# Kernel tuning notes

Hardware: AMD Instinct MI355X
Metric: run time of the kernel (lower is better)

The kernel has to match this reference:

```python
import jax, jax.numpy as jnp
import numpy as np

EPS = 1e-12  # F.normalize eps

def _unfold3(x):
    # x: [B,C,H,W] -> [B, C*9, H*W], matching F.unfold(kernel=3, padding=1)
    B, C, H, W = x.shape
    xp = jnp.pad(x, ((0, 0), (0, 0), (1, 1), (1, 1)))
    pats = jnp.stack([xp[:, :, i:i + H, j:j + W]
                      for i in range(3) for j in range(3)], axis=2)  # [B,C,9,H,W]
    return pats.reshape(B, C * 9, H * W)

def _fold3(t, H, W):
    # inverse of _unfold3 with overlap-add, matching F.fold(kernel=3, padding=1)
    B, CK, L = t.shape
    C = CK // 9
    t = t.reshape(B, C, 3, 3, H, W)
    out = jnp.zeros((B, C, H + 2, W + 2), t.dtype)
    for i in range(3):
        for j in range(3):
            out = out.at[:, :, i:i + H, j:j + W].add(t[:, :, i, j])
    return out[:, :, 1:1 + H, 1:1 + W]

def setup_inputs() -> dict:
    key = jax.random.key(0)
    kV, kK, kQ = jax.random.split(key, 3)
    B, C, H, W = 4, 64, 64, 64
    return {
        'V': jax.random.normal(kV, (B, C, H, W), dtype=jnp.float32),
        'K': jax.random.normal(kK, (B, C, H, W), dtype=jnp.float32),
        'Q': jax.random.normal(kQ, (B, C, H, W), dtype=jnp.float32),
    }

def reference(V, K, Q):
    B, C, H, W = Q.shape
    Qu = _unfold3(Q)  # [B, C9, L]
    Ku = _unfold3(K)  # [B, C9, L]
    # F.normalize along the feature (C*9) axis for both K (after permute dim=2) and Q (dim=1)
    Kn = Ku / jnp.maximum(jnp.linalg.norm(Ku, axis=1, keepdims=True), EPS)
    Qn = Qu / jnp.maximum(jnp.linalg.norm(Qu, axis=1, keepdims=True), EPS)
    # R[b,k,q] = <Kn[b,:,k], Qn[b,:,q]>  -> [B, L, L]
    R = jnp.einsum('bfk,bfq->bkq', Kn, Qn)
    S = jnp.max(R, axis=1)        # [B, L]
    arg = jnp.argmax(R, axis=1)   # [B, L] best key patch per query position
    Vu = _unfold3(V)              # [B, C9, L]
    idx = jnp.broadcast_to(arg[:, None, :], Vu.shape)
    T_unfold = jnp.take_along_axis(Vu, idx, axis=2)  # gather along patch dim
    T = _fold3(T_unfold, H, W) / 9.0                 # [B, C, H, W]
    S = S.reshape(B, 1, H, W)
    return (S, T)
```

## Files before the change

kernel.cpp:

```cpp
#include <hip/hip_runtime.h>
#include <math.h>

#define HW 4096

typedef short bf16x8 __attribute__((ext_vector_type(8)));
typedef float floatx4 __attribute__((ext_vector_type(4)));

__device__ __forceinline__ unsigned short f2bf_rne(float x) {
    unsigned int u = __float_as_uint(x);
    unsigned int r = (u + 0x7FFFu + ((u >> 16) & 1u)) >> 16;
    return (unsigned short)r;
}
__device__ __forceinline__ float bf2f(unsigned short h) {
    return __uint_as_float(((unsigned int)h) << 16);
}

__device__ __forceinline__ void gload_lds16(const void* gptr, void* lptr) {
    auto g = (const __attribute__((address_space(1))) unsigned int*)(unsigned long long)(gptr);
    auto l = (__attribute__((address_space(3))) unsigned int*)(unsigned int)(unsigned long long)(lptr);
    __builtin_amdgcn_global_load_lds(g, l, 16, 0, 0);
}

__global__ __launch_bounds__(256)
void prep_kernel(const float* __restrict__ Q, const float* __restrict__ K,
                 unsigned short* __restrict__ Aq, unsigned short* __restrict__ Bq,
                 float* __restrict__ pix2q, float* __restrict__ pix2k) {
    __shared__ float sT[64][65];
    const int tid = threadIdx.x;
    const int p0 = blockIdx.x * 64;
    const int b = blockIdx.y;
    const int pp = tid >> 2, qt = tid & 3;
    const size_t base = ((size_t)b * 4096 + p0 + pp) * 192;

#pragma unroll
    for (int it = 0; it < 16; ++it) {
        int idx = it * 256 + tid;
        int c = idx >> 6, x = idx & 63;
        sT[c][x] = Q[((size_t)b * 64 + c) * HW + p0 + x];
    }
    __syncthreads();
    {
        float sq = 0.f;
#pragma unroll
        for (int i = 0; i < 16; ++i) {
            int c = qt * 16 + i;
            float x = sT[c][pp];
            sq = fmaf(x, x, sq);
            unsigned short h = f2bf_rne(x);
            unsigned short l = f2bf_rne(x - bf2f(h));
            Aq[base + c] = h;
            Aq[base + 64 + c] = h;
            Aq[base + 128 + c] = l;
        }
        sq += __shfl_xor(sq, 1, 64);
        sq += __shfl_xor(sq, 2, 64);
        if (qt == 0) pix2q[(b << 12) + p0 + pp] = sq;
    }
    __syncthreads();

#pragma unroll
    for (int it = 0; it < 16; ++it) {
        int idx = it * 256 + tid;
        int c = idx >> 6, x = idx & 63;
        sT[c][x] = K[((size_t)b * 64 + c) * HW + p0 + x];
    }
    __syncthreads();
    {
        float sk = 0.f;
#pragma unroll
        for (int i = 0; i < 16; ++i) {
            int c = qt * 16 + i;
            float x = sT[c][pp];
            sk = fmaf(x, x, sk);
            unsigned short h = f2bf_rne(x);
            unsigned short l = f2bf_rne(x - bf2f(h));
            Bq[base + c] = h;
            Bq[base + 64 + c] = l;
            Bq[base + 128 + c] = h;
        }
        sk += __shfl_xor(sk, 1, 64);
        sk += __shfl_xor(sk, 2, 64);
        if (qt == 0) pix2k[(b << 12) + p0 + pp] = sk;
    }
}

__global__ void patchnorm_kernel(const float* __restrict__ pix2q, const float* __restrict__ pix2k,
                                 float* __restrict__ rnq, float* __restrict__ rnk) {
    int idx = blockIdx.x * 256 + threadIdx.x;
    int b = idx >> 12, p = idx & 4095;
    int py = p >> 6, px = p & 63;
    float sq = 0.f, sk = 0.f;
    for (int dy = -1; dy <= 1; ++dy)
        for (int dx = -1; dx <= 1; ++dx) {
            int yy = py + dy, xx = px + dx;
            if ((unsigned)yy < 64u && (unsigned)xx < 64u) {
                int o = (b << 12) + (yy << 6) + xx;
                sq += pix2q[o];
                sk += pix2k[o];
            }
        }
    rnq[idx] = 1.f / fmaxf(sqrtf(sq), 1e-12f);
    rnk[idx] = 1.f / fmaxf(sqrtf(sk), 1e-12f);
}

#define WAITV(n_) asm volatile("s_waitcnt vmcnt(" #n_ ")" ::: "memory")
#define PBAR(n_) do { WAITV(n_); __builtin_amdgcn_s_barrier(); \
                      asm volatile("" ::: "memory"); } while (0)

#define ISSUE_CHUNK(g_) do { \
    const int sg_ = (g_) >> 2, r_ = (g_) & 3; \
    _Pragma("unroll") \
    for (int it_ = 0; it_ < 2; ++it_) { \
        int s16_ = it_ * 256 + tid; \
        int rr_ = s16_ >> 3, pos_ = s16_ & 7, G_ = pos_ ^ (rr_ & 7); \
        gload_lds16(ab + (size_t)(r_ * 64 + rr_) * 384 + sg_ * 128 + G_ * 16, \
                    smem + ((r_ * 64 + rr_) * 8 + pos_) * 16); \
        gload_lds16(bb + (size_t)(r_ * 64 + rr_) * 384 + sg_ * 128 + G_ * 16, \
                    smem + 32768 + ((r_ * 64 + rr_) * 8 + pos_) * 16); \
    } \
} while (0)

#define MFMA_STEP(dy_) do { \
    _Pragma("unroll") \
    for (int kk = 0; kk < 2; ++kk) { \
        bf16x8 af[4], bfr[4]; \
        _Pragma("unroll") \
        for (int mt = 0; mt < 4; ++mt) { \
            int row = (dy_) * 64 + wm * 64 + mt * 16 + m15; \
            int pos = (kk * 4 + quad) ^ (row & 7); \
            af[mt] = *(const bf16x8*)(smem + (row * 8 + pos) * 16); \
        } \
        _Pragma("unroll") \
        for (int nt = 0; nt < 4; ++nt) { \
            int row = (dy_) * 64 + wn * 64 + nt * 16 + m15; \
            int pos = (kk * 4 + quad) ^ (row & 7); \
            bfr[nt] = *(const bf16x8*)(smem + 32768 + (row * 8 + pos) * 16); \
        } \
        __builtin_amdgcn_s_setprio(1); \
        _Pragma("unroll") \
        for (int mt = 0; mt < 4; ++mt) \
            _Pragma("unroll") \
            for (int nt = 0; nt < 4; ++nt) \
                acc[mt][nt] = __builtin_amdgcn_mfma_f32_16x16x32_bf16( \
                    af[mt], bfr[nt], acc[mt][nt], 0, 0, 0); \
        __builtin_amdgcn_s_setprio(0); \
    } \
} while (0)

__global__ __launch_bounds__(256, 2)
void gemm_fused_kernel(const unsigned short* __restrict__ Aq, const unsigned short* __restrict__ Bq,
                       const float* __restrict__ rnkA,
                       float* __restrict__ part_val, int* __restrict__ part_arg) {
    __shared__ __align__(16) char smem[65536];
    const int tid = threadIdx.x;
    const int lane = tid & 63, wid = tid >> 6;
    const int m15 = lane & 15, quad = lane >> 4;
    const int wm = wid & 1, wn = wid >> 1;
    const int k0 = blockIdx.x * 128;
    const int q0 = blockIdx.y * 128;
    const int b = blockIdx.z;
    const char* Aqb = (const char*)(Aq + (size_t)b * 4096 * 192);
    const char* Bqb = (const char*)(Bq + (size_t)b * 4096 * 192);
    const bool aInt = (q0 >= 64) && (q0 <= 4096 - 192);
    const bool bInt = (k0 >= 64) && (k0 <= 4096 - 192);

    floatx4 acc[4][4];
#pragma unroll
    for (int i = 0; i < 4; ++i)
#pragma unroll
        for (int j = 0; j < 4; ++j) acc[i][j] = (floatx4)0.f;

    if (aInt && bInt) {
        const char* ab = Aqb + (size_t)(q0 - 64) * 384;
        const char* bb = Bqb + (size_t)(k0 - 64) * 384;
        ISSUE_CHUNK(0); ISSUE_CHUNK(1); ISSUE_CHUNK(2); ISSUE_CHUNK(3);
        PBAR(8);                                MFMA_STEP(0);
        PBAR(4); ISSUE_CHUNK(4);                MFMA_STEP(1);
        PBAR(4); ISSUE_CHUNK(5);                MFMA_STEP(2);
        PBAR(0); ISSUE_CHUNK(6); ISSUE_CHUNK(7); MFMA_STEP(0);
        PBAR(4); ISSUE_CHUNK(8);                MFMA_STEP(1);
        PBAR(4); ISSUE_CHUNK(9);                MFMA_STEP(2);
        PBAR(0); ISSUE_CHUNK(10); ISSUE_CHUNK(11); MFMA_STEP(0);
        PBAR(4);                                MFMA_STEP(1);
        PBAR(0);                                MFMA_STEP(2);
        __syncthreads();
    } else {
        for (int seg = 0; seg < 3; ++seg) {
            const char* abL = Aqb + (size_t)(q0 - 64) * 384 + seg * 128;
            const char* bbL = Bqb + (size_t)(k0 - 64) * 384 + seg * 128;
            if (aInt) {
#pragma unroll
                for (int it = 0; it < 8; ++it) {
                    int slot = it * 256 + tid;
                    int row = slot >> 3, pos = slot & 7;
                    int G = pos ^ (row & 7);
                    gload_lds16(abL + (size_t)row * 384 + G * 16, smem + slot * 16);
                }
            } else {
#pragma unroll
                for (int it = 0; it < 8; ++it) {
                    int slot = it * 256 + tid;
                    int row = slot >> 3, pos = slot & 7;
                    int G = pos ^ (row & 7);
                    uint4 v = make_uint4(0u, 0u, 0u, 0u);
                    if ((unsigned)(q0 - 64 + row) < 4096u)
                        v = *(const uint4*)(abL + (size_t)row * 384 + G * 16);
                    *(uint4*)(smem + slot * 16) = v;
                }
            }
            if (bInt) {
#pragma unroll
                for (int it = 0; it < 8; ++it) {
                    int slot = it * 256 + tid;
                    int row = slot >> 3, pos = slot & 7;
                    int G = pos ^ (row & 7);
                    gload_lds16(bbL + (size_t)row * 384 + G * 16, smem + 32768 + slot * 16);
                }
            } else {
#pragma unroll
                for (int it = 0; it < 8; ++it) {
                    int slot = it * 256 + tid;
                    int row = slot >> 3, pos = slot & 7;
                    int G = pos ^ (row & 7);
                    uint4 v = make_uint4(0u, 0u, 0u, 0u);
                    if ((unsigned)(k0 - 64 + row) < 4096u)
                        v = *(const uint4*)(bbL + (size_t)row * 384 + G * 16);
                    *(uint4*)(smem + 32768 + slot * 16) = v;
                }
            }
            __syncthreads();
            MFMA_STEP(0); MFMA_STEP(1); MFMA_STEP(2);
            __syncthreads();
        }
    }

    float* Csh = (float*)smem;
    float* bvs = (float*)(smem + 34816);
    int*   bas = (int*)(smem + 35840);
    const int q_l = tid & 63;
    const int qr = tid >> 6;
    const int c0 = qr * 32;
    const float4 zero4 = make_float4(0.f, 0.f, 0.f, 0.f);

#pragma unroll
    for (int h = 0; h < 2; ++h) {
        if (h) __syncthreads();
        if (wm == h) {
#pragma unroll
            for (int mt = 0; mt < 4; ++mt)
#pragma unroll
                for (int nt = 0; nt < 4; ++nt)
#pragma unroll
                    for (int j = 0; j < 4; ++j)
                        Csh[(mt * 16 + quad * 4 + j) * 133 + wn * 64 + nt * 16 + m15] =
                            acc[mt][nt][j];
        }
        __syncthreads();

        const bool qm = q_l > 0;
        const bool qp = q_l < 63;
        const float* rC = Csh + q_l * 133;
        const float* rM = Csh + (q_l - 1) * 133;
        const float* rP = Csh + (q_l + 1) * 133;
        float4 prevm = (qm && c0 > 0) ? *(const float4*)&rM[c0 - 4] : zero4;
        float4 rpj   = qp ? *(const float4*)&rP[c0] : zero4;
        float bv = -INFINITY;
        int ba = 0;
#pragma unroll
        for (int j = 0; j < 8; ++j) {
            int c = c0 + 4 * j;
            float4 cen = *(const float4*)&rC[c];
            float4 rm4 = qm ? *(const float4*)&rM[c] : zero4;
            float4 rp1 = (qp && (c + 4) < 128) ? *(const float4*)&rP[c + 4] : zero4;
            float4 o;
            o.x = cen.x + (((c & 63) != 0) ? prevm.w : 0.f) + rpj.y;
            o.y = cen.y + rm4.x + rpj.z;
            o.z = cen.z + rm4.y + rpj.w;
            o.w = cen.w + rm4.z + ((((c + 3) & 63) != 63) ? rp1.x : 0.f);
            float4 rk = *(const float4*)&rnkA[(b << 12) + k0 + c];
            float v0 = o.x * rk.x; if (v0 > bv) { bv = v0; ba = k0 + c + 0; }
            float v1 = o.y * rk.y; if (v1 > bv) { bv = v1; ba = k0 + c + 1; }
            float v2 = o.z * rk.z; if (v2 > bv) { bv = v2; ba = k0 + c + 2; }
            float v3 = o.w * rk.w; if (v3 > bv) { bv = v3; ba = k0 + c + 3; }
            prevm = rm4;
            rpj = rp1;
        }
        bvs[(qr << 6) + q_l] = bv;
        bas[(qr << 6) + q_l] = ba;
        __syncthreads();
        if (tid < 64) {
            float v = bvs[tid];
            int a = bas[tid];
#pragma unroll
            for (int s = 1; s < 4; ++s) {
                float v2 = bvs[(s << 6) + tid];
                if (v2 > v) { v = v2; a = bas[(s << 6) + tid]; }
            }
            int q = q0 + h * 64 + tid;
            part_val[(((b << 5) + blockIdx.x) << 12) + q] = v;
            part_arg[(((b << 5) + blockIdx.x) << 12) + q] = a;
        }
    }
}

__global__ __launch_bounds__(256)
void gatherS_kernel(const float* __restrict__ V,
                    const float* __restrict__ part_val, const int* __restrict__ part_arg,
                    const float* __restrict__ rnqA,
                    float* __restrict__ S_out, float* __restrict__ T_out) {
    __shared__ int sArg[192];
    const int y = blockIdx.x, b = blockIdx.y;
    const int tid = threadIdx.x;
    if (tid < 192) {
        int r = tid >> 6, x = tid & 63;
        int yy = y - 1 + r;
        int a = 0;
        if ((unsigned)yy < 64u) {
            int base = (b << 17) + (yy << 6) + x;
            float bv = -INFINITY; int ba = 0;
#pragma unroll 8
            for (int s = 0; s < 32; ++s) {
                float v = part_val[base + (s << 12)];
                int aa = part_arg[base + (s << 12)];
                if (v > bv) { bv = v; ba = aa; }
            }
            a = ba;
            if (r == 1) {
                int idx = (b << 12) + (yy << 6) + x;
                S_out[idx] = bv * rnqA[idx];
            }
        }
        sArg[tid] = a;
    }
    __syncthreads();

    const int x = tid & 63, cq = tid >> 6;
    int off[9];
#pragma unroll
    for (int t = 0; t < 9; ++t) {
        int dy = t / 3 - 1, dx = t % 3 - 1;
        int qy = y - dy, qx = x - dx;
        int o = -1;
        if ((unsigned)qy < 64u && (unsigned)qx < 64u) {
            int a = sArg[(1 - dy) * 64 + qx];
            int sy = (a >> 6) + dy, sx = (a & 63) + dx;
            if ((unsigned)sy < 64u && (unsigned)sx < 64u) o = (sy << 6) + sx;
        }
        off[t] = o;
    }
    const float* Vb = V + (size_t)b * 64 * HW;
    float* Tb = T_out + (size_t)b * 64 * HW + (y << 6) + x;
    for (int ci = 0; ci < 16; ++ci) {
        int c = cq * 16 + ci;
        const float* Vc = Vb + (size_t)c * HW;
        float acc = 0.f;
#pragma unroll
        for (int t = 0; t < 9; ++t)
            acc += (off[t] >= 0) ? Vc[off[t]] : 0.f;
        Tb[(size_t)c * HW] = acc * (1.f / 9.f);
    }
}

extern "C" void kernel_launch(void* const* d_in, const int* in_sizes, int n_in,
                              void* d_out, int out_size, void* d_ws, size_t ws_size,
                              hipStream_t stream) {
    const float* V = (const float*)d_in[0];
    const float* K = (const float*)d_in[1];
    const float* Q = (const float*)d_in[2];
    float* S_out = (float*)d_out;
    float* T_out = S_out + 4 * HW;

    char* ws = (char*)d_ws;
    float* pix2q = (float*)(ws + 0);
    float* pix2k = (float*)(ws + 65536);
    float* rnq   = (float*)(ws + 131072);
    float* rnk   = (float*)(ws + 196608);
    float* part_val = (float*)(ws + 262144);
    int*   part_arg = (int*)(ws + 8650752);
    unsigned short* Aq = (unsigned short*)(ws + 17039360);
    unsigned short* Bq = (unsigned short*)(ws + 23330816);

    prep_kernel<<<dim3(64, 4), 256, 0, stream>>>(Q, K, Aq, Bq, pix2q, pix2k);
    patchnorm_kernel<<<64, 256, 0, stream>>>(pix2q, pix2k, rnq, rnk);
    gemm_fused_kernel<<<dim3(32, 32, 4), 256, 0, stream>>>(Aq, Bq, rnk, part_val, part_arg);
    gatherS_kernel<<<dim3(64, 4), 256, 0, stream>>>(V, part_val, part_arg, rnq, S_out, T_out);
}
```

Before: 220.2 us.

## Cache A fragments in registers across dy shifts and remap block order

The GEMM main loop is restructured so A-tile fragments loaded in the first K-segment stay in registers (afc) and are reused in the second segment, which only loads B. LDS becomes a ring of 8KB slots with a new issue order and wait counts, growing shared memory to 72KB. Block indices are also swizzled so neighbouring workgroups share q-tiles, which should improve L2 reuse. The cost is more register pressure from holding 24 bf16x8 fragments, which may lower occupancy under launch_bounds(256,2), plus more complex slot bookkeeping.

```diff
diff --git a/kernel.cpp b/kernel.cpp
--- a/kernel.cpp
+++ b/kernel.cpp
@@ -107,43 +107,74 @@
 #define PBAR(n_) do { WAITV(n_); __builtin_amdgcn_s_barrier(); \
                       asm volatile("" ::: "memory"); } while (0)
 
-#define ISSUE_CHUNK(g_) do { \
-    const int sg_ = (g_) >> 2, r_ = (g_) & 3; \
+#define ISSUE_A(c_, sg_, slot_) do { \
+    const char* g_ = Aqb + (size_t)(q0 - 64 + (c_) * 64) * 384 + (sg_) * 128; \
+    gload_lds16(g_ + g0off, smem + (slot_) * 8192 + l0off); \
+    gload_lds16(g_ + g1off, smem + (slot_) * 8192 + l1off); \
+} while (0)
+#define ISSUE_B(c_, sg_, slot_) do { \
+    const char* g_ = Bqb + (size_t)(k0 - 64 + (c_) * 64) * 384 + (sg_) * 128; \
+    gload_lds16(g_ + g0off, smemB + (slot_) * 8192 + l0off); \
+    gload_lds16(g_ + g1off, smemB + (slot_) * 8192 + l1off); \
+} while (0)
+
+#define MM16(af_, bfr_) do { \
+    __builtin_amdgcn_s_setprio(1); \
     _Pragma("unroll") \
-    for (int it_ = 0; it_ < 2; ++it_) { \
-        int s16_ = it_ * 256 + tid; \
-        int rr_ = s16_ >> 3, pos_ = s16_ & 7, G_ = pos_ ^ (rr_ & 7); \
-        gload_lds16(ab + (size_t)(r_ * 64 + rr_) * 384 + sg_ * 128 + G_ * 16, \
-                    smem + ((r_ * 64 + rr_) * 8 + pos_) * 16); \
-        gload_lds16(bb + (size_t)(r_ * 64 + rr_) * 384 + sg_ * 128 + G_ * 16, \
-                    smem + 32768 + ((r_ * 64 + rr_) * 8 + pos_) * 16); \
-    } \
-} while (0)
-
-#define MFMA_STEP(dy_) do { \
+    for (int mt = 0; mt < 4; ++mt) \
+        _Pragma("unroll") \
+        for (int nt = 0; nt < 4; ++nt) \
+            acc[mt][nt] = __builtin_amdgcn_mfma_f32_16x16x32_bf16( \
+                (af_)[mt], (bfr_)[nt], acc[mt][nt], 0, 0, 0); \
+    __builtin_amdgcn_s_setprio(0); \
+} while (0)
+
+#define STEP_S0(D_) do { \
+    const char* As_ = smem + (wm + (D_)) * 8192; \
+    const char* Bs_ = smemB + (wn + (D_)) * 8192; \
     _Pragma("unroll") \
     for (int kk = 0; kk < 2; ++kk) { \
+        const int pk_ = kk ? posK1 : posK0; \
+        bf16x8 bfr[4]; \
+        _Pragma("unroll") \
+        for (int mt = 0; mt < 4; ++mt) \
+            afc[(D_)][kk][mt] = *(const bf16x8*)(As_ + mt * 2048 + rowB + pk_); \
+        _Pragma("unroll") \
+        for (int nt = 0; nt < 4; ++nt) \
+            bfr[nt] = *(const bf16x8*)(Bs_ + nt * 2048 + rowB + pk_); \
+        MM16(afc[(D_)][kk], bfr); \
+    } \
+} while (0)
+
+#define STEP_S1(D_) do { \
+    const int xb_ = wn + (D_); \
+    const char* Bs_ = smemB + (xb_ ? (xb_ - 1) : 4) * 8192; \
+    _Pragma("unroll") \
+    for (int kk = 0; kk < 2; ++kk) { \
+        const int pk_ = kk ? posK1 : posK0; \
+        bf16x8 bfr[4]; \
+        _Pragma("unroll") \
+        for (int nt = 0; nt < 4; ++nt) \
+            bfr[nt] = *(const bf16x8*)(Bs_ + nt * 2048 + rowB + pk_); \
+        MM16(afc[(D_)][kk], bfr); \
+    } \
+} while (0)
+
+#define STEP_S2(D_) do { \
+    const int xa_ = wm + (D_), xb_ = wn + (D_); \
+    const char* As_ = smem + (xa_ ? (xa_ - 1) : 3) * 8192; \
+    const char* Bs_ = smemB + (xb_ < 2 ? xb_ + 3 : xb_ - 2) * 8192; \
+    _Pragma("unroll") \
+    for (int kk = 0; kk < 2; ++kk) { \
+        const int pk_ = kk ? posK1 : posK0; \
         bf16x8 af[4], bfr[4]; \
         _Pragma("unroll") \
-        for (int mt = 0; mt < 4; ++mt) { \
-            int row = (dy_) * 64 + wm * 64 + mt * 16 + m15; \
-            int pos = (kk * 4 + quad) ^ (row & 7); \
-            af[mt] = *(const bf16x8*)(smem + (row * 8 + pos) * 16); \
-        } \
-        _Pragma("unroll") \
-        for (int nt = 0; nt < 4; ++nt) { \
-            int row = (dy_) * 64 + wn * 64 + nt * 16 + m15; \
-            int pos = (kk * 4 + quad) ^ (row & 7); \
-            bfr[nt] = *(const bf16x8*)(smem + 32768 + (row * 8 + pos) * 16); \
-        } \
-        __builtin_amdgcn_s_setprio(1); \
-        _Pragma("unroll") \
         for (int mt = 0; mt < 4; ++mt) \
-            _Pragma("unroll") \
-            for (int nt = 0; nt < 4; ++nt) \
-                acc[mt][nt] = __builtin_amdgcn_mfma_f32_16x16x32_bf16( \
-                    af[mt], bfr[nt], acc[mt][nt], 0, 0, 0); \
-        __builtin_amdgcn_s_setprio(0); \
+            af[mt] = *(const bf16x8*)(As_ + mt * 2048 + rowB + pk_); \
+        _Pragma("unroll") \
+        for (int nt = 0; nt < 4; ++nt) \
+            bfr[nt] = *(const bf16x8*)(Bs_ + nt * 2048 + rowB + pk_); \
+        MM16(af, bfr); \
     } \
 } while (0)
 
@@ -151,38 +182,55 @@
 void gemm_fused_kernel(const unsigned short* __restrict__ Aq, const unsigned short* __restrict__ Bq,
                        const float* __restrict__ rnkA,
                        float* __restrict__ part_val, int* __restrict__ part_arg) {
-    __shared__ __align__(16) char smem[65536];
+    __shared__ __align__(16) char smem[73728];
+    char* const smemB = smem + 32768;
     const int tid = threadIdx.x;
     const int lane = tid & 63, wid = tid >> 6;
     const int m15 = lane & 15, quad = lane >> 4;
     const int wm = wid & 1, wn = wid >> 1;
-    const int k0 = blockIdx.x * 128;
-    const int q0 = blockIdx.y * 128;
+    const int f = blockIdx.x + (blockIdx.y << 5);
+    const int o = ((f & 7) << 7) + (f >> 3);
+    const int kt = o & 31, qt = o >> 5;
+    const int k0 = kt << 7;
+    const int q0 = qt << 7;
     const int b = blockIdx.z;
     const char* Aqb = (const char*)(Aq + (size_t)b * 4096 * 192);
     const char* Bqb = (const char*)(Bq + (size_t)b * 4096 * 192);
     const bool aInt = (q0 >= 64) && (q0 <= 4096 - 192);
     const bool bInt = (k0 >= 64) && (k0 <= 4096 - 192);
 
+    const int rr0 = tid >> 3, ps = tid & 7;
+    const int g0off = rr0 * 384 + (ps ^ (rr0 & 7)) * 16;
+    const int l0off = tid * 16;
+    const int rr1 = (256 + tid) >> 3;
+    const int g1off = rr1 * 384 + (ps ^ (rr1 & 7)) * 16;
+    const int l1off = (256 + tid) * 16;
+    const int rowB = m15 * 128;
+    const int posK0 = (quad ^ (m15 & 7)) * 16;
+    const int posK1 = ((4 + quad) ^ (m15 & 7)) * 16;
+
     floatx4 acc[4][4];
 #pragma unroll
     for (int i = 0; i < 4; ++i)
 #pragma unroll
         for (int j = 0; j < 4; ++j) acc[i][j] = (floatx4)0.f;
 
+    bf16x8 afc[3][2][4];
+
     if (aInt && bInt) {
-        const char* ab = Aqb + (size_t)(q0 - 64) * 384;
-        const char* bb = Bqb + (size_t)(k0 - 64) * 384;
-        ISSUE_CHUNK(0); ISSUE_CHUNK(1); ISSUE_CHUNK(2); ISSUE_CHUNK(3);
-        PBAR(8);                                MFMA_STEP(0);
-        PBAR(4); ISSUE_CHUNK(4);                MFMA_STEP(1);
-        PBAR(4); ISSUE_CHUNK(5);                MFMA_STEP(2);
-        PBAR(0); ISSUE_CHUNK(6); ISSUE_CHUNK(7); MFMA_STEP(0);
-        PBAR(4); ISSUE_CHUNK(8);                MFMA_STEP(1);
-        PBAR(4); ISSUE_CHUNK(9);                MFMA_STEP(2);
-        PBAR(0); ISSUE_CHUNK(10); ISSUE_CHUNK(11); MFMA_STEP(0);
-        PBAR(4);                                MFMA_STEP(1);
-        PBAR(0);                                MFMA_STEP(2);
+        ISSUE_A(0, 0, 0); ISSUE_A(1, 0, 1); ISSUE_B(0, 0, 0); ISSUE_B(1, 0, 1);
+        ISSUE_A(2, 0, 2); ISSUE_B(2, 0, 2); ISSUE_A(3, 0, 3); ISSUE_B(3, 0, 3);
+        ISSUE_B(0, 1, 4);
+        PBAR(10);                                   STEP_S0(0);
+        PBAR(6);  ISSUE_B(1, 1, 0); ISSUE_A(1, 2, 0); STEP_S0(1);
+        PBAR(6);  ISSUE_B(2, 1, 1); ISSUE_A(2, 2, 1); STEP_S0(2);
+        PBAR(6);  ISSUE_B(3, 1, 2); ISSUE_B(0, 0, 3);
+                  ISSUE_A(0, 2, 3); ISSUE_A(3, 2, 2); STEP_S1(0);
+        PBAR(10); ISSUE_B(1, 0, 4);                 STEP_S1(1);
+        PBAR(8);  ISSUE_B(2, 0, 0);                 STEP_S1(2);
+        PBAR(2);  ISSUE_B(3, 0, 1);                 STEP_S2(0);
+        PBAR(2);                                    STEP_S2(1);
+        PBAR(0);                                    STEP_S2(2);
         __syncthreads();
     } else {
         for (int seg = 0; seg < 3; ++seg) {
@@ -214,7 +262,7 @@
                     int slot = it * 256 + tid;
                     int row = slot >> 3, pos = slot & 7;
                     int G = pos ^ (row & 7);
-                    gload_lds16(bbL + (size_t)row * 384 + G * 16, smem + 32768 + slot * 16);
+                    gload_lds16(bbL + (size_t)row * 384 + G * 16, smemB + slot * 16);
                 }
             } else {
 #pragma unroll
@@ -225,11 +273,11 @@
                     uint4 v = make_uint4(0u, 0u, 0u, 0u);
                     if ((unsigned)(k0 - 64 + row) < 4096u)
                         v = *(const uint4*)(bbL + (size_t)row * 384 + G * 16);
-                    *(uint4*)(smem + 32768 + slot * 16) = v;
+                    *(uint4*)(smemB + slot * 16) = v;
                 }
             }
             __syncthreads();
-            MFMA_STEP(0); MFMA_STEP(1); MFMA_STEP(2);
+            STEP_S0(0); STEP_S0(1); STEP_S0(2);
             __syncthreads();
         }
     }
@@ -272,16 +320,16 @@
             float4 cen = *(const float4*)&rC[c];
             float4 rm4 = qm ? *(const float4*)&rM[c] : zero4;
             float4 rp1 = (qp && (c + 4) < 128) ? *(const float4*)&rP[c + 4] : zero4;
-            float4 o;
-            o.x = cen.x + (((c & 63) != 0) ? prevm.w : 0.f) + rpj.y;
-            o.y = cen.y + rm4.x + rpj.z;
-            o.z = cen.z + rm4.y + rpj.w;
-            o.w = cen.w + rm4.z + ((((c + 3) & 63) != 63) ? rp1.x : 0.f);
+            float4 o4;
+            o4.x = cen.x + (((c & 63) != 0) ? prevm.w : 0.f) + rpj.y;
+            o4.y = cen.y + rm4.x + rpj.z;
+            o4.z = cen.z + rm4.y + rpj.w;
+            o4.w = cen.w + rm4.z + ((((c + 3) & 63) != 63) ? rp1.x : 0.f);
             float4 rk = *(const float4*)&rnkA[(b << 12) + k0 + c];
-            float v0 = o.x * rk.x; if (v0 > bv) { bv = v0; ba = k0 + c + 0; }
-            float v1 = o.y * rk.y; if (v1 > bv) { bv = v1; ba = k0 + c + 1; }
-            float v2 = o.z * rk.z; if (v2 > bv) { bv = v2; ba = k0 + c + 2; }
-            float v3 = o.w * rk.w; if (v3 > bv) { bv = v3; ba = k0 + c + 3; }
+            float v0 = o4.x * rk.x; if (v0 > bv) { bv = v0; ba = k0 + c + 0; }
+            float v1 = o4.y * rk.y; if (v1 > bv) { bv = v1; ba = k0 + c + 1; }
+            float v2 = o4.z * rk.z; if (v2 > bv) { bv = v2; ba = k0 + c + 2; }
+            float v3 = o4.w * rk.w; if (v3 > bv) { bv = v3; ba = k0 + c + 3; }
             prevm = rm4;
             rpj = rp1;
         }
@@ -297,8 +345,8 @@
                 if (v2 > v) { v = v2; a = bas[(s << 6) + tid]; }
             }
             int q = q0 + h * 64 + tid;
-            part_val[(((b << 5) + blockIdx.x) << 12) + q] = v;
-            part_arg[(((b << 5) + blockIdx.x) << 12) + q] = a;
+            part_val[(((b << 5) + kt) << 12) + q] = v;
+            part_arg[(((b << 5) + kt) << 12) + q] = a;
         }
     }
 }
```

New measurement: 211.4 us. -4.0%, faster.
